# Kernel optimization log

Hardware: AMD Instinct MI355X
Metric: run time of the kernel (lower is better)

Reference implementation:

```python
import jax, jax.numpy as jnp
import numpy as np

EPS = 1e-6  # torch.nn.CosineSimilarity eps


def setup_inputs() -> dict:
    key = jax.random.key(0)
    k1, k2, k3, k4 = jax.random.split(key, 4)
    B, S, I, H, P = 16, 512, 512, 512, 16
    hidden = jax.random.normal(k1, (B, S, I), dtype=jnp.float32)
    # per-prototype linear weights (no bias); torch Linear stores (out, in)
    W1 = jax.random.normal(k2, (P, H, I), dtype=jnp.float32) / np.sqrt(I)
    W2 = jax.random.normal(k3, (P, H, H), dtype=jnp.float32) / np.sqrt(H)
    protos = jax.random.normal(k4, (P, H), dtype=jnp.float32)  # torch.randn(1,H) per proto
    return {"hidden": hidden, "W1": W1, "W2": W2, "protos": protos}


def reference(hidden, W1, W2, protos):
    # Batched version of the per-prototype loop:
    # layer1: ReLU(hidden @ W1[p].T) -> [B,S,P,H]
    h1 = jax.nn.relu(jnp.einsum("bsi,phi->bsph", hidden, W1))
    # layer2: ReLU(h1 @ W2[p].T) -> [B,S,P,H]
    h2 = jax.nn.relu(jnp.einsum("bsph,pgh->bspg", h1, W2))
    # cosine similarity along feature dim vs. each prototype vector
    dot = jnp.einsum("bsph,ph->bsp", h2, protos)
    xn = jnp.maximum(jnp.linalg.norm(h2, axis=-1), EPS)          # [B,S,P]
    pn = jnp.maximum(jnp.linalg.norm(protos, axis=-1), EPS)      # [P]
    cos_scores = dot / (xn * pn)                                  # [B,S,P]
    return cos_scores
```

## Files before the change

### kernel.cpp

```cpp
#include <hip/hip_runtime.h>
#include <hip/hip_bf16.h>

#define R_TOT 8192
#define DIM   512
#define NP    16
#define EPSV  1e-6f

typedef __bf16 bf16x8 __attribute__((ext_vector_type(8)));
typedef float  f32x4  __attribute__((ext_vector_type(4)));

__device__ __forceinline__ unsigned int f2bf(float f) {
  unsigned int u = __float_as_uint(f);
  return (u + 0x7FFFu + ((u >> 16) & 1u)) >> 16;
}
__device__ __forceinline__ unsigned int pack2(float a, float b) {
  return f2bf(a) | (f2bf(b) << 16);
}

__global__ void cvt_x_kernel(const float* __restrict__ X, unsigned short* __restrict__ Xb) {
  int t   = blockIdx.x * 256 + threadIdx.x;
  int row = t >> 6;
  int c   = t & 63;
  const float4* src = (const float4*)(X + (size_t)row * DIM + c * 8);
  float4 f0 = src[0], f1 = src[1];
  uint4 o;
  o.x = pack2(f0.x, f0.y);
  o.y = pack2(f0.z, f0.w);
  o.z = pack2(f1.x, f1.y);
  o.w = pack2(f1.z, f1.w);
  *(uint4*)(Xb + (size_t)row * DIM + 8 * (c ^ (row & 7))) = o;
}

__global__ void pack_w_kernel(const float* __restrict__ W, unsigned short* __restrict__ Wp) {
  int t  = blockIdx.x * 256 + threadIdx.x;
  int l  = t & 63;
  int kk = (t >> 6) & 15;
  int mt = (t >> 10) & 31;
  int p  = t >> 15;
  int row = mt * 16 + (l & 15);
  int k0  = 32 * kk + 8 * (l >> 4);
  const float4* s = (const float4*)(W + ((size_t)p * DIM + row) * DIM + k0);
  float4 f0 = s[0], f1 = s[1];
  uint4 o;
  o.x = pack2(f0.x, f0.y);
  o.y = pack2(f0.z, f0.w);
  o.z = pack2(f1.x, f1.y);
  o.w = pack2(f1.z, f1.w);
  *(uint4*)(Wp + (size_t)t * 8) = o;
}

__global__ void proto_norm_kernel(const float* __restrict__ protos, float* __restrict__ pn) {
  int p = blockIdx.x;
  int l = threadIdx.x;
  float ss = 0.f;
  #pragma unroll
  for (int k = 0; k < DIM / 64; ++k) {
    float v = protos[p * DIM + k * 64 + l];
    ss += v * v;
  }
  #pragma unroll
  for (int m = 32; m >= 1; m >>= 1) ss += __shfl_xor(ss, m, 64);
  if (l == 0) pn[p] = fmaxf(sqrtf(ss), EPSV);
}

__device__ __forceinline__ void gemm_stage(const unsigned short* tile,
                                           const unsigned short* __restrict__ Wpk,
                                           f32x4 acc[2][4],
                                           int l, int l15, int q) {
  for (int kk = 0; kk < 16; ++kk) {
    bf16x8 a[2], b[4];
    #pragma unroll
    for (int mi = 0; mi < 2; ++mi)
      a[mi] = *(const bf16x8*)(Wpk + (size_t)mi * 8192 + kk * 512 + l * 8);
    #pragma unroll
    for (int nt = 0; nt < 4; ++nt) {
      int row  = nt * 16 + l15;
      int boff = (64 * kk + 16 * q) ^ ((row & 7) << 4);
      b[nt] = *(const bf16x8*)((const char*)tile + row * 1024 + boff);
    }
    #pragma unroll
    for (int mi = 0; mi < 2; ++mi)
      #pragma unroll
      for (int nt = 0; nt < 4; ++nt)
        acc[mi][nt] = __builtin_amdgcn_mfma_f32_16x16x32_bf16(a[mi], b[nt], acc[mi][nt], 0, 0, 0);
  }
}

__global__ __launch_bounds__(1024) void fused_kernel(
    const unsigned short* __restrict__ Xb,
    const unsigned short* __restrict__ W1p,
    const unsigned short* __restrict__ W2p,
    const float* __restrict__ protos,
    const float* __restrict__ pn,
    float* __restrict__ out) {
  __shared__ unsigned short tile[64 * DIM];
  __shared__ float red[16][64][2];

  const int raw = blockIdx.x;
  const int bid = (raw & 7) * 256 + (raw >> 3);
  const int p   = bid >> 7;
  const int r0  = (bid & 127) << 6;
  const int tid = threadIdx.x;
  const int w   = tid >> 6;
  const int l   = tid & 63;
  const int l15 = l & 15;
  const int q   = l >> 4;

  {
    const uint4* g = (const uint4*)(Xb + (size_t)r0 * DIM);
    uint4* s = (uint4*)tile;
    #pragma unroll
    for (int it = 0; it < 4; ++it) s[tid + it * 1024] = g[tid + it * 1024];
  }
  __syncthreads();

  f32x4 acc[2][4];
  #pragma unroll
  for (int mi = 0; mi < 2; ++mi)
    #pragma unroll
    for (int nt = 0; nt < 4; ++nt) acc[mi][nt] = (f32x4){0.f, 0.f, 0.f, 0.f};

  gemm_stage(tile, W1p + ((size_t)p * 32 + 2 * w) * 8192, acc, l, l15, q);

  __syncthreads();

  #pragma unroll
  for (int mi = 0; mi < 2; ++mi)
    #pragma unroll
    for (int nt = 0; nt < 4; ++nt) {
      int token = nt * 16 + l15;
      int featb = ((2 * w + mi) * 16 + q * 4) * 2;
      uint2 pk;
      pk.x = pack2(fmaxf(acc[mi][nt][0], 0.f), fmaxf(acc[mi][nt][1], 0.f));
      pk.y = pack2(fmaxf(acc[mi][nt][2], 0.f), fmaxf(acc[mi][nt][3], 0.f));
      *(uint2*)((char*)tile + token * 1024 + (featb ^ ((token & 7) << 4))) = pk;
    }
  __syncthreads();

  #pragma unroll
  for (int mi = 0; mi < 2; ++mi)
    #pragma unroll
    for (int nt = 0; nt < 4; ++nt) acc[mi][nt] = (f32x4){0.f, 0.f, 0.f, 0.f};

  gemm_stage(tile, W2p + ((size_t)p * 32 + 2 * w) * 8192, acc, l, l15, q);

  float4 pv[2];
  #pragma unroll
  for (int mi = 0; mi < 2; ++mi)
    pv[mi] = *(const float4*)(protos + p * DIM + (2 * w + mi) * 16 + q * 4);

  #pragma unroll
  for (int nt = 0; nt < 4; ++nt) {
    float d = 0.f, ssq = 0.f;
    #pragma unroll
    for (int mi = 0; mi < 2; ++mi)
      #pragma unroll
      for (int j = 0; j < 4; ++j) {
        float h = fmaxf(acc[mi][nt][j], 0.f);
        d   += h * ((const float*)&pv[mi])[j];
        ssq += h * h;
      }
    d   += __shfl_xor(d, 16, 64);
    d   += __shfl_xor(d, 32, 64);
    ssq += __shfl_xor(ssq, 16, 64);
    ssq += __shfl_xor(ssq, 32, 64);
    if (q == 0) {
      red[w][nt * 16 + l15][0] = d;
      red[w][nt * 16 + l15][1] = ssq;
    }
  }
  __syncthreads();

  if (tid < 64) {
    float d = 0.f, ssq = 0.f;
    #pragma unroll
    for (int ww = 0; ww < 16; ++ww) {
      d   += red[ww][tid][0];
      ssq += red[ww][tid][1];
    }
    float xn = fmaxf(sqrtf(ssq), EPSV);
    out[(size_t)(r0 + tid) * NP + p] = d / (xn * pn[p]);
  }
}

extern "C" void kernel_launch(void* const* d_in, const int* in_sizes, int n_in,
                              void* d_out, int out_size, void* d_ws, size_t ws_size,
                              hipStream_t stream) {
  const float* X      = (const float*)d_in[0];
  const float* W1     = (const float*)d_in[1];
  const float* W2     = (const float*)d_in[2];
  const float* protos = (const float*)d_in[3];
  float* out = (float*)d_out;

  unsigned short* Xb  = (unsigned short*)d_ws;
  unsigned short* W1p = Xb  + (size_t)R_TOT * DIM;
  unsigned short* W2p = W1p + (size_t)NP * DIM * DIM;
  float* pn = (float*)(W2p + (size_t)NP * DIM * DIM);

  cvt_x_kernel<<<2048, 256, 0, stream>>>(X, Xb);
  pack_w_kernel<<<2048, 256, 0, stream>>>(W1, W1p);
  pack_w_kernel<<<2048, 256, 0, stream>>>(W2, W2p);
  proto_norm_kernel<<<NP, 64, 0, stream>>>(protos, pn);
  fused_kernel<<<2048, 1024, 0, stream>>>(Xb, W1p, W2p, protos, pn, out);
}
```

Measured before the change: 156.1 us.

## Switch GEMM stages from 16x16x32 to 32x32x16 bf16 MFMA tiles

```diff
diff --git a/kernel.cpp b/kernel.cpp
--- a/kernel.cpp
+++ b/kernel.cpp
@@ -7,7 +7,7 @@
 #define EPSV  1e-6f
 
 typedef __bf16 bf16x8 __attribute__((ext_vector_type(8)));
-typedef float  f32x4  __attribute__((ext_vector_type(4)));
+typedef float  f32x16 __attribute__((ext_vector_type(16)));
 
 __device__ __forceinline__ unsigned int f2bf(float f) {
   unsigned int u = __float_as_uint(f);
@@ -15,6 +15,12 @@
 }
 __device__ __forceinline__ unsigned int pack2(float a, float b) {
   return f2bf(a) | (f2bf(b) << 16);
+}
+__device__ __forceinline__ f32x16 zero16() {
+  f32x16 z;
+  #pragma unroll
+  for (int i = 0; i < 16; ++i) z[i] = 0.f;
+  return z;
 }
 
 __global__ void cvt_x_kernel(const float* __restrict__ X, unsigned short* __restrict__ Xb) {
@@ -34,11 +40,11 @@
 __global__ void pack_w_kernel(const float* __restrict__ W, unsigned short* __restrict__ Wp) {
   int t  = blockIdx.x * 256 + threadIdx.x;
   int l  = t & 63;
-  int kk = (t >> 6) & 15;
-  int mt = (t >> 10) & 31;
+  int kk = (t >> 6) & 31;
+  int mt = (t >> 11) & 15;
   int p  = t >> 15;
-  int row = mt * 16 + (l & 15);
-  int k0  = 32 * kk + 8 * (l >> 4);
+  int row = mt * 32 + (l & 31);
+  int k0  = 16 * kk + 8 * (l >> 5);
   const float4* s = (const float4*)(W + ((size_t)p * DIM + row) * DIM + k0);
   float4 f0 = s[0], f1 = s[1];
   uint4 o;
@@ -63,26 +69,20 @@
   if (l == 0) pn[p] = fmaxf(sqrtf(ss), EPSV);
 }
 
-__device__ __forceinline__ void gemm_stage(const unsigned short* tile,
-                                           const unsigned short* __restrict__ Wpk,
-                                           f32x4 acc[2][4],
-                                           int l, int l15, int q) {
-  for (int kk = 0; kk < 16; ++kk) {
-    bf16x8 a[2], b[4];
-    #pragma unroll
-    for (int mi = 0; mi < 2; ++mi)
-      a[mi] = *(const bf16x8*)(Wpk + (size_t)mi * 8192 + kk * 512 + l * 8);
-    #pragma unroll
-    for (int nt = 0; nt < 4; ++nt) {
-      int row  = nt * 16 + l15;
-      int boff = (64 * kk + 16 * q) ^ ((row & 7) << 4);
-      b[nt] = *(const bf16x8*)((const char*)tile + row * 1024 + boff);
-    }
-    #pragma unroll
-    for (int mi = 0; mi < 2; ++mi)
-      #pragma unroll
-      for (int nt = 0; nt < 4; ++nt)
-        acc[mi][nt] = __builtin_amdgcn_mfma_f32_16x16x32_bf16(a[mi], b[nt], acc[mi][nt], 0, 0, 0);
+__device__ __forceinline__ void gemm_stage32(const unsigned short* tile,
+                                             const unsigned short* __restrict__ Wpk,
+                                             f32x16 acc[2],
+                                             int l, int l31, int h) {
+  #pragma unroll
+  for (int kk = 0; kk < 32; ++kk) {
+    bf16x8 a = *(const bf16x8*)(Wpk + kk * 512 + l * 8);
+    #pragma unroll
+    for (int nt = 0; nt < 2; ++nt) {
+      int token = nt * 32 + l31;
+      int boff  = (32 * kk + 16 * h) ^ ((token & 7) << 4);
+      bf16x8 b = *(const bf16x8*)((const char*)tile + token * 1024 + boff);
+      acc[nt] = __builtin_amdgcn_mfma_f32_32x32x16_bf16(a, b, acc[nt], 0, 0, 0);
+    }
   }
 }
 
@@ -103,8 +103,8 @@
   const int tid = threadIdx.x;
   const int w   = tid >> 6;
   const int l   = tid & 63;
-  const int l15 = l & 15;
-  const int q   = l >> 4;
+  const int l31 = l & 31;
+  const int h   = l >> 5;
 
   {
     const uint4* g = (const uint4*)(Xb + (size_t)r0 * DIM);
@@ -114,59 +114,54 @@
   }
   __syncthreads();
 
-  f32x4 acc[2][4];
-  #pragma unroll
-  for (int mi = 0; mi < 2; ++mi)
-    #pragma unroll
-    for (int nt = 0; nt < 4; ++nt) acc[mi][nt] = (f32x4){0.f, 0.f, 0.f, 0.f};
-
-  gemm_stage(tile, W1p + ((size_t)p * 32 + 2 * w) * 8192, acc, l, l15, q);
-
-  __syncthreads();
-
-  #pragma unroll
-  for (int mi = 0; mi < 2; ++mi)
-    #pragma unroll
-    for (int nt = 0; nt < 4; ++nt) {
-      int token = nt * 16 + l15;
-      int featb = ((2 * w + mi) * 16 + q * 4) * 2;
+  f32x16 acc[2];
+  acc[0] = zero16();
+  acc[1] = zero16();
+
+  gemm_stage32(tile, W1p + ((size_t)p * 16 + w) * 16384, acc, l, l31, h);
+
+  __syncthreads();
+
+  #pragma unroll
+  for (int nt = 0; nt < 2; ++nt) {
+    int token = nt * 32 + l31;
+    #pragma unroll
+    for (int g = 0; g < 4; ++g) {
       uint2 pk;
-      pk.x = pack2(fmaxf(acc[mi][nt][0], 0.f), fmaxf(acc[mi][nt][1], 0.f));
-      pk.y = pack2(fmaxf(acc[mi][nt][2], 0.f), fmaxf(acc[mi][nt][3], 0.f));
+      pk.x = pack2(fmaxf(acc[nt][4 * g + 0], 0.f), fmaxf(acc[nt][4 * g + 1], 0.f));
+      pk.y = pack2(fmaxf(acc[nt][4 * g + 2], 0.f), fmaxf(acc[nt][4 * g + 3], 0.f));
+      int featb = 64 * w + 16 * g + 8 * h;
       *(uint2*)((char*)tile + token * 1024 + (featb ^ ((token & 7) << 4))) = pk;
     }
-  __syncthreads();
-
-  #pragma unroll
-  for (int mi = 0; mi < 2; ++mi)
-    #pragma unroll
-    for (int nt = 0; nt < 4; ++nt) acc[mi][nt] = (f32x4){0.f, 0.f, 0.f, 0.f};
-
-  gemm_stage(tile, W2p + ((size_t)p * 32 + 2 * w) * 8192, acc, l, l15, q);
-
-  float4 pv[2];
-  #pragma unroll
-  for (int mi = 0; mi < 2; ++mi)
-    pv[mi] = *(const float4*)(protos + p * DIM + (2 * w + mi) * 16 + q * 4);
-
-  #pragma unroll
-  for (int nt = 0; nt < 4; ++nt) {
+  }
+  __syncthreads();
+
+  acc[0] = zero16();
+  acc[1] = zero16();
+
+  gemm_stage32(tile, W2p + ((size_t)p * 16 + w) * 16384, acc, l, l31, h);
+
+  float4 pv[4];
+  #pragma unroll
+  for (int g = 0; g < 4; ++g)
+    pv[g] = *(const float4*)(protos + p * DIM + 32 * w + 8 * g + 4 * h);
+
+  #pragma unroll
+  for (int nt = 0; nt < 2; ++nt) {
     float d = 0.f, ssq = 0.f;
     #pragma unroll
-    for (int mi = 0; mi < 2; ++mi)
+    for (int g = 0; g < 4; ++g)
       #pragma unroll
       for (int j = 0; j < 4; ++j) {
-        float h = fmaxf(acc[mi][nt][j], 0.f);
-        d   += h * ((const float*)&pv[mi])[j];
-        ssq += h * h;
+        float hv = fmaxf(acc[nt][4 * g + j], 0.f);
+        d   += hv * ((const float*)&pv[g])[j];
+        ssq += hv * hv;
       }
-    d   += __shfl_xor(d, 16, 64);
     d   += __shfl_xor(d, 32, 64);
-    ssq += __shfl_xor(ssq, 16, 64);
     ssq += __shfl_xor(ssq, 32, 64);
-    if (q == 0) {
-      red[w][nt * 16 + l15][0] = d;
-      red[w][nt * 16 + l15][1] = ssq;
+    if (l < 32) {
+      red[w][nt * 32 + l31][0] = d;
+      red[w][nt * 32 + l31][1] = ssq;
     }
   }
   __syncthreads();
```

Result: slower. 177.2 us (+13.6%).
